# Kernel optimization log

Hardware: AMD Instinct MI355X
Metric: run time of the kernel (lower is better)

Reference implementation:

```python
import jax, jax.numpy as jnp
import numpy as np

K_TOP = 10
DEPTH = 1
N_RULES = 2
N_HOPS = 2
IS_REVERSED = (False, True)


def setup_inputs() -> dict:
    key = jax.random.key(0)
    ks = jax.random.split(key, 11)
    B, E, N, F = 16, 256, 1024, 2048
    return {
        'rel': jax.random.normal(ks[0], (B, E), jnp.float32),
        'arg1': jax.random.normal(ks[1], (B, E), jnp.float32),
        'arg2': jax.random.normal(ks[2], (B, E), jnp.float32),
        'fact_rel': jax.random.normal(ks[3], (B, F, E), jnp.float32),
        'fact_arg1': jax.random.normal(ks[4], (B, F, E), jnp.float32),
        'fact_arg2': jax.random.normal(ks[5], (B, F, E), jnp.float32),
        'nb_facts': jax.random.randint(ks[6], (B,), 1, F + 1),
        'entity_embeddings': jax.random.normal(ks[7], (B, N, E), jnp.float32),
        'nb_entities': jax.random.randint(ks[8], (B,), 1, N + 1),
        'W': jax.random.normal(ks[9], (N_RULES, N_HOPS, E, E), jnp.float32) / np.sqrt(E),
        'b': jnp.zeros((N_RULES, N_HOPS, E), jnp.float32),
    }


def _kernel_scores(q, f):
    # q: [B, M, E], f: [B, F, E] -> Gaussian kernel exp(-0.5*||q-f||^2): [B, M, F]
    d = (jnp.sum(q * q, -1)[..., None] + jnp.sum(f * f, -1)[:, None, :]
         - 2.0 * jnp.einsum('bme,bfe->bmf', q, f))
    return jnp.exp(-0.5 * jnp.maximum(d, 0.0))


def kb_score(rel, arg1, arg2, fact_rel, fact_arg1, fact_arg2, nb_facts):
    # BatchNeuralKB.score: product of per-component kernels, mask padded facts, max over facts.
    B, F, E = fact_rel.shape
    M = rel.shape[0] // B
    r = rel.reshape(B, M, E); a1 = arg1.reshape(B, M, E); a2 = arg2.reshape(B, M, E)
    s = (_kernel_scores(r, fact_rel) * _kernel_scores(a1, fact_arg1)
         * _kernel_scores(a2, fact_arg2))                       # [B, M, F]
    mask = jnp.arange(F)[None, None, :] < nb_facts[:, None, None]
    s = jnp.where(mask, s, 0.0)
    return jnp.max(s, axis=-1).reshape(-1)                      # [B*M]


def prove(rel, arg1, arg2, fact_rel, fact_arg1, fact_arg2, nb_facts,
          entity_embeddings, W, b, depth):
    scores_0 = kb_score(rel, arg1, arg2, fact_rel, fact_arg1, fact_arg2, nb_facts)
    if depth == 0:
        return scores_0
    B, E = rel.shape
    N = entity_embeddings.shape[1]
    global_res = None
    for rule_idx in range(N_RULES):
        is_rev = IS_REVERSED[rule_idx]
        hop_rel_lst = [rel @ W[rule_idx, h] + b[rule_idx, h] for h in range(N_HOPS)]
        sources, scores = arg1, None
        for hop_idx, hop_rel in enumerate(hop_rel_lst, start=1):
            sources_2d = sources.reshape(-1, E)
            nb_branches = sources_2d.shape[0] // B
            hop_rel_2d = jnp.repeat(hop_rel, nb_branches, axis=0)   # [B*br, E]
            if hop_idx < N_HOPS:
                ent_rep = jnp.repeat(entity_embeddings, nb_branches, axis=0)  # [B*br, N, E]
                all_ent_2d = ent_rep.reshape(-1, E)                  # [B*br*N, E]
                new_src_2d = jnp.repeat(sources_2d, N, axis=0)       # [B*br*N, E]
                hop_rel_big = jnp.repeat(hop_rel_2d, N, axis=0)
                na1, na2 = (all_ent_2d, new_src_2d) if is_rev else (new_src_2d, all_ent_2d)
                new_scores = prove(hop_rel_big, na1, na2, fact_rel, fact_arg1,
                                   fact_arg2, nb_facts, entity_embeddings, W, b,
                                   depth - 1).reshape(-1, N)         # [B*br, N]
                k = min(K_TOP, N)
                z_scores, z_idx = jax.lax.top_k(new_scores, k)       # [B*br, k]
                z_emb = jnp.take_along_axis(ent_rep, z_idx[..., None], axis=1)  # [B*br, k, E]
                sources = z_emb.reshape(-1, E)
                z1d = z_scores.reshape(-1)
                scores = z1d if scores is None else jnp.minimum(z1d, jnp.repeat(scores, k))
            else:
                arg2_2d = jnp.repeat(arg2, nb_branches, axis=0)
                na1, na2 = (arg2_2d, sources_2d) if is_rev else (sources_2d, arg2_2d)
                z1d = prove(hop_rel_2d, na1, na2, fact_rel, fact_arg1, fact_arg2,
                            nb_facts, entity_embeddings, W, b, depth - 1)
                scores = z1d if scores is None else jnp.minimum(z1d, scores)
        res = jnp.max(scores.reshape(B, -1), axis=1)
        global_res = res if global_res is None else jnp.maximum(global_res, res)
    return jnp.maximum(scores_0, global_res)


def reference(rel, arg1, arg2, fact_rel, fact_arg1, fact_arg2, nb_facts,
              entity_embeddings, nb_entities, W, b):
    return prove(rel, arg1, arg2, fact_rel, fact_arg1, fact_arg2, nb_facts,
                 entity_embeddings, W, b, depth=DEPTH)
```

## Files before the change

### kernel.cpp

```cpp
#include <hip/hip_runtime.h>
#include <math.h>

#define E 256
#define KTOP 10
#define NY 8
#define NINF (-__builtin_huge_valf())

typedef __attribute__((ext_vector_type(4))) float f32x4;
typedef __attribute__((ext_vector_type(2))) long i64x2;

__device__ inline float wsum(float v) {
    v += __shfl_xor(v, 1, 64);
    v += __shfl_xor(v, 2, 64);
    v += __shfl_xor(v, 4, 64);
    v += __shfl_xor(v, 8, 64);
    v += __shfl_xor(v, 16, 64);
    v += __shfl_xor(v, 32, 64);
    return v;
}

__device__ inline float wmax(float v) {
    v = fmaxf(v, __shfl_xor(v, 1, 64));
    v = fmaxf(v, __shfl_xor(v, 2, 64));
    v = fmaxf(v, __shfl_xor(v, 4, 64));
    v = fmaxf(v, __shfl_xor(v, 8, 64));
    v = fmaxf(v, __shfl_xor(v, 16, 64));
    v = fmaxf(v, __shfl_xor(v, 32, 64));
    return v;
}

__device__ inline float dot4(float4 a, float4 b) {
    return a.x * b.x + a.y * b.y + a.z * b.z + a.w * b.w;
}

__device__ inline void atomicMaxF(float* addr, float v) {
    atomicMax((unsigned int*)addr, __float_as_uint(v));
}

__device__ inline unsigned char f2fp8(float x) {
    unsigned u = __float_as_uint(x);
    unsigned s = (u >> 24) & 0x80u;
    int e = (int)((u >> 23) & 0xFF) - 127;
    unsigned m = u & 0x7FFFFFu;
    if (e < -9) return (unsigned char)s;
    if (e > 8) return (unsigned char)(s | 0x7E);
    if (e >= -6) {
        unsigned mant = m >> 20;
        unsigned rest = m & 0xFFFFFu;
        if (rest > 0x80000u || (rest == 0x80000u && (mant & 1))) mant++;
        unsigned v = (((unsigned)(e + 7)) << 3) + mant;
        if (v > 0x7Eu) v = 0x7Eu;
        return (unsigned char)(s | v);
    }
    int rs = 20 + (-6 - e);
    unsigned full = 0x800000u | m;
    unsigned mant = full >> rs;
    unsigned rem = full & ((1u << rs) - 1u);
    unsigned half = 1u << (rs - 1);
    if (rem > half || (rem == half && (mant & 1))) mant++;
    if (mant >= 8u) return (unsigned char)(s | 0x08u);
    return (unsigned char)(s | mant);
}

__device__ inline int tile_off(int e0, int col) {
    return ((e0 >> 6) << 10) + (col << 6) + (((e0 & 31) >> 3) << 4) +
           (((e0 >> 5) & 1) << 3) + (e0 & 7);
}

__global__ void k_hoprel(const float* __restrict__ rel, const float* __restrict__ arg1,
                         const float* __restrict__ arg2, const float* __restrict__ W,
                         const float* __restrict__ bias, float* __restrict__ hr,
                         float* __restrict__ nhr, float* __restrict__ nrel,
                         float* __restrict__ na1, float* __restrict__ na2, int B) {
    int b = blockIdx.x, rh = blockIdx.y;
    int j = threadIdx.x;
    __shared__ float relS[E];
    __shared__ float red[4];
    __shared__ float red2[4];
    relS[j] = rel[b * E + j];
    __syncthreads();
    const float* Wp = W + (size_t)rh * E * E;
    float acc = bias[rh * E + j];
#pragma unroll 8
    for (int e = 0; e < E; ++e) acc = fmaf(relS[e], Wp[e * E + j], acc);
    hr[((size_t)rh * B + b) * E + j] = acc;
    float s = wsum(acc * acc);
    int wave = j >> 6;
    if ((j & 63) == 0) red[wave] = s;
    float x = 0.f;
    if (rh == 0) x = relS[j];
    else if (rh == 1) x = arg1[b * E + j];
    else if (rh == 2) x = arg2[b * E + j];
    float s2 = wsum(x * x);
    if ((j & 63) == 0) red2[wave] = s2;
    __syncthreads();
    if (j == 0) {
        nhr[rh * B + b] = red[0] + red[1] + red[2] + red[3];
        if (rh < 3) {
            float nv = red2[0] + red2[1] + red2[2] + red2[3];
            (rh == 0 ? nrel : (rh == 1 ? na1 : na2))[b] = nv;
        }
    }
}

__global__ void k_prep_ent(const float* __restrict__ ent, unsigned char* __restrict__ entb,
                           unsigned char* __restrict__ entt, float* __restrict__ ne_,
                           int BN, int N) {
    int row = blockIdx.x * 4 + (threadIdx.x >> 6);
    if (row >= BN) return;
    int lane = threadIdx.x & 63;
    float4 v = ((const float4*)(ent + (size_t)row * E))[lane];
    float s = wsum(dot4(v, v));
    if (lane == 0) ne_[row] = s;
    uchar4 o;
    o.x = f2fp8(v.x); o.y = f2fp8(v.y); o.z = f2fp8(v.z); o.w = f2fp8(v.w);
    ((uchar4*)(entb + (size_t)row * E))[lane] = o;
    int b = row / N, n = row % N;
    size_t tbase = ((size_t)b * (N >> 4) + (n >> 4)) * 4096;
    *(uchar4*)(entt + tbase + tile_off(lane * 4, n & 15)) = o;
}

__global__ __launch_bounds__(256) void k_fused(
    const float* __restrict__ rel, const float* __restrict__ arg1,
    const float* __restrict__ arg2, const float* __restrict__ frel,
    const float* __restrict__ fa1, const float* __restrict__ fa2,
    const int* __restrict__ nbf, const float* __restrict__ hr,
    const float* __restrict__ nhr, const float* __restrict__ nrel,
    const float* __restrict__ na1, const float* __restrict__ na2,
    float* __restrict__ lw1, float* __restrict__ lw2, float* __restrict__ s0log,
    float* __restrict__ nf1, float* __restrict__ nf2,
    unsigned char* __restrict__ fa1b, unsigned char* __restrict__ fa2b,
    int B, int F) {
    int b = blockIdx.y;
    int lane = threadIdx.x & 63, wave = threadIdx.x >> 6;
    int f = blockIdx.x * 4 + wave;
    size_t bf = (size_t)b * F + f;
    float4 qrel = ((const float4*)(rel + (size_t)b * E))[lane];
    float4 qa1  = ((const float4*)(arg1 + (size_t)b * E))[lane];
    float4 qa2  = ((const float4*)(arg2 + (size_t)b * E))[lane];
    float4 qh00 = ((const float4*)(hr + ((size_t)0 * B + b) * E))[lane];
    float4 qh01 = ((const float4*)(hr + ((size_t)1 * B + b) * E))[lane];
    float4 qh10 = ((const float4*)(hr + ((size_t)2 * B + b) * E))[lane];
    float4 qh11 = ((const float4*)(hr + ((size_t)3 * B + b) * E))[lane];
    float4 v  = ((const float4*)(frel + bf * E))[lane];
    float4 v1 = ((const float4*)(fa1 + bf * E))[lane];
    float4 v2 = ((const float4*)(fa2 + bf * E))[lane];
    size_t tbase = ((size_t)b * (F >> 4) + (f >> 4)) * 4096;
    int off = tile_off(lane * 4, f & 15);
    uchar4 c1, c2;
    c1.x = f2fp8(v1.x); c1.y = f2fp8(v1.y); c1.z = f2fp8(v1.z); c1.w = f2fp8(v1.w);
    c2.x = f2fp8(v2.x); c2.y = f2fp8(v2.y); c2.z = f2fp8(v2.z); c2.w = f2fp8(v2.w);
    *(uchar4*)(fa1b + tbase + off) = c1;
    *(uchar4*)(fa2b + tbase + off) = c2;
    float d_rel  = wsum(dot4(v, qrel));
    float d_h00  = wsum(dot4(v, qh00));
    float d_h01  = wsum(dot4(v, qh01));
    float d_h10  = wsum(dot4(v, qh10));
    float d_h11  = wsum(dot4(v, qh11));
    float n_fr   = wsum(dot4(v, v));
    float d_a1f1 = wsum(dot4(v1, qa1));
    float d_a2f1 = wsum(dot4(v1, qa2));
    float n_f1   = wsum(dot4(v1, v1));
    float d_a1f2 = wsum(dot4(v2, qa1));
    float d_a2f2 = wsum(dot4(v2, qa2));
    float n_f2   = wsum(dot4(v2, v2));
    if (lane == 0) {
        bool msk = (f < nbf[b]);
        float rrel  = fmaxf(nrel[b] + n_fr - 2.f * d_rel, 0.f);
        float rh00  = fmaxf(nhr[0 * B + b] + n_fr - 2.f * d_h00, 0.f);
        float rh01  = fmaxf(nhr[1 * B + b] + n_fr - 2.f * d_h01, 0.f);
        float rh10  = fmaxf(nhr[2 * B + b] + n_fr - 2.f * d_h10, 0.f);
        float rh11  = fmaxf(nhr[3 * B + b] + n_fr - 2.f * d_h11, 0.f);
        float ra1f1 = fmaxf(na1[b] + n_f1 - 2.f * d_a1f1, 0.f);
        float ra2f1 = fmaxf(na2[b] + n_f1 - 2.f * d_a2f1, 0.f);
        float ra1f2 = fmaxf(na1[b] + n_f2 - 2.f * d_a1f2, 0.f);
        float ra2f2 = fmaxf(na2[b] + n_f2 - 2.f * d_a2f2, 0.f);
        nf1[bf] = n_f1;
        nf2[bf] = n_f2;
        lw1[bf]                 = msk ? -0.5f * (rh00 + ra1f1) : NINF;
        lw1[(size_t)B * F + bf] = msk ? -0.5f * (rh10 + ra1f2) : NINF;
        lw2[bf]                 = msk ? -0.5f * (rh01 + ra2f2) : NINF;
        lw2[(size_t)B * F + bf] = msk ? -0.5f * (rh11 + ra2f1) : NINF;
        s0log[bf] = msk ? -0.5f * (rrel + ra1f1 + ra2f2) : NINF;
    }
}

__global__ void k_s0red(const float* __restrict__ s0log, float* __restrict__ out,
                        int B, int F) {
    int b = blockIdx.x;
    int tid = threadIdx.x, lane = tid & 63, wave = tid >> 6;
    float m = NINF;
    for (int f = tid; f < F; f += 256) m = fmaxf(m, s0log[(size_t)b * F + f]);
    m = wmax(m);
    __shared__ float red[4];
    if (lane == 0) red[wave] = m;
    __syncthreads();
    if (tid == 0) out[b] = expf(fmaxf(fmaxf(red[0], red[1]), fmaxf(red[2], red[3])));
}

__global__ __launch_bounds__(256, 4) void k_hop1m(
    const unsigned char* __restrict__ entt, const unsigned char* __restrict__ fa1b,
    const unsigned char* __restrict__ fa2b, const float* __restrict__ nf1,
    const float* __restrict__ nf2, const float* __restrict__ ne,
    const float* __restrict__ lw1, float* __restrict__ nsc_part, int B, int N, int F) {
    int L = blockIdx.x;
    int xcd = L & 7, s = L >> 3;
    int b = ((s >> 7) << 3) | xcd;
    int inner = s & 127;
    int r = inner >> 6, nb = (inner >> 3) & 7, fs = inner & 7;
    int BR = nb * 128;
    int F0 = fs * 256;
    const unsigned char* factb = (r == 0) ? fa2b : fa1b;
    const float* nfp = ((r == 0) ? nf2 : nf1) + (size_t)b * F;
    const float* w = lw1 + ((size_t)r * B + b) * F;
    const float* nep = ne + (size_t)b * N;

    __shared__ unsigned char bT[2][4096];

    int tid = threadIdx.x, lane = tid & 63, wave = tid >> 6;
    int lr = lane & 15, lk = lane >> 4;
    int row0 = BR + wave * 32;

    const unsigned char* At = entt + (size_t)b * N * E;
    long areg[2][8];
#pragma unroll
    for (int m = 0; m < 2; ++m) {
        const unsigned char* p = At + (size_t)((row0 >> 4) + m) * 4096 + lr * 64 + lk * 16;
#pragma unroll
        for (int g = 0; g < 4; ++g) {
            i64x2 vv = *(const i64x2*)(p + g * 1024);
            areg[m][2 * g] = vv.x;
            areg[m][2 * g + 1] = vv.y;
        }
    }
    float nh[2][4];
#pragma unroll
    for (int m = 0; m < 2; ++m)
#pragma unroll
        for (int j = 0; j < 4; ++j)
            nh[m][j] = -0.5f * nep[row0 + m * 16 + lk * 4 + j];
    float lwa[16], gfa[16];
#pragma unroll
    for (int t = 0; t < 16; ++t) {
        int fcol = F0 + t * 16 + lr;
        lwa[t] = w[fcol];
        gfa[t] = fmaf(-0.5f, nfp[fcol], lwa[t]);
    }
    float vmax[2][4];
#pragma unroll
    for (int m = 0; m < 2; ++m)
#pragma unroll
        for (int j = 0; j < 4; ++j) vmax[m][j] = NINF;

    const unsigned char* Bt = factb + (size_t)b * F * E + (size_t)(F0 >> 4) * 4096;
#define STG(buf, t)                                                            \
    __builtin_amdgcn_global_load_lds(                                          \
        (const __attribute__((address_space(1))) void*)(Bt + (size_t)(t) * 4096 + \
                                                        wave * 1024 + lane * 16), \
        (__attribute__((address_space(3))) void*)&bT[buf][wave * 1024], 16, 0, 0)

    STG(0, 0);
    __syncthreads();
#pragma unroll
    for (int t = 0; t < 16; ++t) {
        int cur = t & 1;
        if (t < 15) STG(cur ^ 1, t + 1);
        long bfr[8];
#pragma unroll
        for (int g = 0; g < 4; ++g) {
            i64x2 vv = *(const i64x2*)&bT[cur][g * 1024 + lr * 64 + lk * 16];
            bfr[2 * g] = vv.x;
            bfr[2 * g + 1] = vv.y;
        }
        f32x4 acc0 = {0.f, 0.f, 0.f, 0.f}, acc1 = {0.f, 0.f, 0.f, 0.f};
#pragma unroll
        for (int kb = 0; kb < 8; ++kb) {
            acc0 = __builtin_amdgcn_mfma_f32_16x16x32_fp8_fp8(areg[0][kb], bfr[kb],
                                                              acc0, 0, 0, 0);
            acc1 = __builtin_amdgcn_mfma_f32_16x16x32_fp8_fp8(areg[1][kb], bfr[kb],
                                                              acc1, 0, 0, 0);
        }
#pragma unroll
        for (int j = 0; j < 4; ++j) {
            vmax[0][j] = fmaxf(vmax[0][j], fminf(acc0[j] + gfa[t] + nh[0][j], lwa[t]));
            vmax[1][j] = fmaxf(vmax[1][j], fminf(acc1[j] + gfa[t] + nh[1][j], lwa[t]));
        }
        __syncthreads();
    }
#undef STG

#pragma unroll
    for (int m = 0; m < 2; ++m)
#pragma unroll
        for (int j = 0; j < 4; ++j) {
            float v = vmax[m][j];
            v = fmaxf(v, __shfl_xor(v, 1, 64));
            v = fmaxf(v, __shfl_xor(v, 2, 64));
            v = fmaxf(v, __shfl_xor(v, 4, 64));
            v = fmaxf(v, __shfl_xor(v, 8, 64));
            if (lr == 0) {
                int row = row0 + m * 16 + lk * 4 + j;
                nsc_part[(size_t)fs * (2 * (size_t)B * N) +
                         ((size_t)r * B + b) * N + row] = v;
            }
        }
}

__global__ __launch_bounds__(256) void k_topk(const float* __restrict__ nsc_part,
                                              float* __restrict__ zval,
                                              int* __restrict__ zidx, int B, int N) {
    int b = blockIdx.x, r = blockIdx.y;
    int tid = threadIdx.x, lane = tid & 63, wave = tid >> 6;
    size_t rbN = ((size_t)r * B + b) * N;
    size_t ystr = 2 * (size_t)B * N;
    const float4* p0 = (const float4*)(nsc_part + rbN) + tid;
    float4 m = *p0;
#pragma unroll
    for (int y = 1; y < NY; ++y) {
        float4 t = *(const float4*)((const float*)p0 + (size_t)y * ystr);
        m.x = fmaxf(m.x, t.x); m.y = fmaxf(m.y, t.y);
        m.z = fmaxf(m.z, t.z); m.w = fmaxf(m.w, t.w);
    }
    float v0 = expf(m.x), v1 = expf(m.y), v2 = expf(m.z), v3 = expf(m.w);
    int base = tid * 4;
    __shared__ float rv[4];
    __shared__ int ri[4];
    for (int t = 0; t < KTOP; ++t) {
        float bv = v0; int bi = base;
        if (v1 > bv) { bv = v1; bi = base + 1; }
        if (v2 > bv) { bv = v2; bi = base + 2; }
        if (v3 > bv) { bv = v3; bi = base + 3; }
#pragma unroll
        for (int off = 32; off > 0; off >>= 1) {
            float ov = __shfl_xor(bv, off, 64);
            int oi = __shfl_xor(bi, off, 64);
            if (ov > bv || (ov == bv && oi < bi)) { bv = ov; bi = oi; }
        }
        if (lane == 0) { rv[wave] = bv; ri[wave] = bi; }
        __syncthreads();
        float fb = rv[0]; int fi = ri[0];
#pragma unroll
        for (int wv = 1; wv < 4; ++wv) {
            float ov = rv[wv]; int oi = ri[wv];
            if (ov > fb || (ov == fb && oi < fi)) { fb = ov; fi = oi; }
        }
        if (tid == 0) {
            zval[((size_t)r * B + b) * KTOP + t] = fb;
            zidx[((size_t)r * B + b) * KTOP + t] = fi;
        }
        int off = fi - base;
        v0 = (off == 0) ? -2.f : v0;
        v1 = (off == 1) ? -2.f : v1;
        v2 = (off == 2) ? -2.f : v2;
        v3 = (off == 3) ? -2.f : v3;
        __syncthreads();
    }
}

__global__ __launch_bounds__(256) void k_hop2m(
    const unsigned char* __restrict__ entb, const unsigned char* __restrict__ fa1b,
    const unsigned char* __restrict__ fa2b, const float* __restrict__ nf1,
    const float* __restrict__ nf2, const float* __restrict__ ne,
    const float* __restrict__ lw2, const int* __restrict__ zidx,
    float* __restrict__ h2part, int B, int N, int F) {
    int L = blockIdx.x;
    int xcd = L & 7, s = L >> 3;
    int b = ((s >> 4) << 3) | xcd;
    int inner = s & 15;
    int r = inner >> 3, c = inner & 7;
    const unsigned char* factb = (r == 0) ? fa1b : fa2b;
    const float* nfp = ((r == 0) ? nf1 : nf2) + (size_t)b * F;
    const float* w = lw2 + ((size_t)r * B + b) * F;
    int tid = threadIdx.x, lane = tid & 63, wave = tid >> 6;
    int lr = lane & 15, lk = lane >> 4;
    __shared__ unsigned char aLds[32 * 16 * 8];
    __shared__ float snrm[16];
    for (int ci = tid; ci < 512; ci += 256) {
        int row = ci & 15, kc = ci >> 4;
        long vv = 0;
        if (row < KTOP) {
            int idx = zidx[((size_t)r * B + b) * KTOP + row];
            vv = *(const long*)(entb + ((size_t)b * N + idx) * E + kc * 8);
        }
        *(long*)&aLds[(size_t)ci * 8] = vv;
    }
    if (tid < 16) {
        float nv = 0.f;
        if (tid < KTOP) {
            int idx = zidx[((size_t)r * B + b) * KTOP + tid];
            nv = ne[(size_t)b * N + idx];
        }
        snrm[tid] = nv;
    }
    __syncthreads();
    long afr[8];
#pragma unroll
    for (int kb = 0; kb < 8; ++kb)
        afr[kb] = *(const long*)&aLds[((kb * 4 + lk) * 16 + lr) * 8];
    float nhs[4];
#pragma unroll
    for (int j = 0; j < 4; ++j) nhs[j] = -0.5f * snrm[lk * 4 + j];
    int fbase = c * (F >> 3) + wave * (F >> 5);
    float vmax[4] = {NINF, NINF, NINF, NINF};
    const unsigned char* Bb = factb + (size_t)b * F * E;
#pragma unroll
    for (int n = 0; n < 4; ++n) {
        int fcol = fbase + n * 16;
        const unsigned char* p = Bb + (size_t)(fcol >> 4) * 4096 + lr * 64 + lk * 16;
        long bfr[8];
#pragma unroll
        for (int g = 0; g < 4; ++g) {
            i64x2 vv = *(const i64x2*)(p + g * 1024);
            bfr[2 * g] = vv.x;
            bfr[2 * g + 1] = vv.y;
        }
        f32x4 acc = {0.f, 0.f, 0.f, 0.f};
#pragma unroll
        for (int kb = 0; kb < 8; ++kb)
            acc = __builtin_amdgcn_mfma_f32_16x16x32_fp8_fp8(afr[kb], bfr[kb], acc,
                                                             0, 0, 0);
        float lwf = w[fcol + lr];
        float gf = fmaf(-0.5f, nfp[fcol + lr], lwf);
#pragma unroll
        for (int j = 0; j < 4; ++j)
            vmax[j] = fmaxf(vmax[j], fminf(acc[j] + gf + nhs[j], lwf));
    }
#pragma unroll
    for (int j = 0; j < 4; ++j) {
        float v = vmax[j];
        v = fmaxf(v, __shfl_xor(v, 1, 64));
        v = fmaxf(v, __shfl_xor(v, 2, 64));
        v = fmaxf(v, __shfl_xor(v, 4, 64));
        v = fmaxf(v, __shfl_xor(v, 8, 64));
        int sidx = lk * 4 + j;
        if (lr == 0 && sidx < KTOP)
            h2part[(((size_t)r * B + b) * KTOP + sidx) * 32 + c * 4 + wave] = v;
    }
}

__global__ void k_hop2c(const float* __restrict__ h2part, const float* __restrict__ zval,
                        float* __restrict__ out, int B) {
    int i = blockIdx.x * 256 + threadIdx.x;
    int n = 2 * B * KTOP;
    if (i < n) {
        int b = (i / KTOP) % B;
        float m = NINF;
#pragma unroll
        for (int c2 = 0; c2 < 32; ++c2) m = fmaxf(m, h2part[(size_t)i * 32 + c2]);
        float sc = fminf(expf(m), zval[i]);
        atomicMaxF(&out[b], sc);
    }
}

extern "C" void kernel_launch(void* const* d_in, const int* in_sizes, int n_in,
                              void* d_out, int out_size, void* d_ws, size_t ws_size,
                              hipStream_t stream) {
    const float* rel = (const float*)d_in[0];
    const float* arg1 = (const float*)d_in[1];
    const float* arg2 = (const float*)d_in[2];
    const float* frel = (const float*)d_in[3];
    const float* fa1 = (const float*)d_in[4];
    const float* fa2 = (const float*)d_in[5];
    const int* nbf = (const int*)d_in[6];
    const float* ent = (const float*)d_in[7];
    const float* W = (const float*)d_in[9];
    const float* bias = (const float*)d_in[10];
    int B = in_sizes[0] / E;
    int F = in_sizes[3] / (B * E);
    int N = in_sizes[7] / (B * E);
    float* out = (float*)d_out;

    float* ws = (float*)d_ws;
    size_t o = 0;
    float* hr = ws + o;   o += (size_t)4 * B * E;
    float* nhr = ws + o;  o += (size_t)4 * B;
    float* nrel = ws + o; o += B;
    float* na1 = ws + o;  o += B;
    float* na2 = ws + o;  o += B * 2;
    float* nf1 = ws + o;  o += (size_t)B * F;
    float* nf2 = ws + o;  o += (size_t)B * F;
    float* ne_ = ws + o;  o += (size_t)B * N;
    float* lw1 = ws + o;  o += (size_t)2 * B * F;
    float* lw2 = ws + o;  o += (size_t)2 * B * F;
    float* zval = ws + o; o += (size_t)2 * B * KTOP;
    int* zidx = (int*)(ws + o); o += (size_t)2 * B * KTOP;
    float* s0log = ws + o; o += (size_t)B * F;
    float* h2part = ws + o; o += (size_t)2 * B * KTOP * 32;
    float* nsc_part = ws + o; o += (size_t)NY * 2 * B * N;
    unsigned char* fa1b = (unsigned char*)(ws + o); o += (size_t)B * F * E / 4;
    unsigned char* fa2b = (unsigned char*)(ws + o); o += (size_t)B * F * E / 4;
    unsigned char* entb = (unsigned char*)(ws + o); o += (size_t)B * N * E / 4;
    unsigned char* entt = (unsigned char*)(ws + o); o += (size_t)B * N * E / 4;

    k_hoprel<<<dim3(B, 4), dim3(E), 0, stream>>>(rel, arg1, arg2, W, bias, hr, nhr,
                                                 nrel, na1, na2, B);
    k_prep_ent<<<dim3((B * N + 3) / 4), dim3(256), 0, stream>>>(ent, entb, entt, ne_,
                                                                B * N, N);
    k_fused<<<dim3(F / 4, B), dim3(256), 0, stream>>>(
        rel, arg1, arg2, frel, fa1, fa2, nbf, hr, nhr, nrel, na1, na2, lw1, lw2,
        s0log, nf1, nf2, fa1b, fa2b, B, F);
    k_s0red<<<dim3(B), dim3(256), 0, stream>>>(s0log, out, B, F);
    k_hop1m<<<dim3(2048), dim3(256), 0, stream>>>(entt, fa1b, fa2b, nf1, nf2, ne_, lw1,
                                                  nsc_part, B, N, F);
    k_topk<<<dim3(B, 2), dim3(256), 0, stream>>>(nsc_part, zval, zidx, B, N);
    k_hop2m<<<dim3(256), dim3(256), 0, stream>>>(entb, fa1b, fa2b, nf1, nf2, ne_, lw2,
                                                 zidx, h2part, B, N, F);
    k_hop2c<<<dim3((2 * B * KTOP + 255) / 256), dim3(256), 0, stream>>>(h2part, zval,
                                                                        out, B);
}
```

Before: 107.0 us.

## Reorder fp8 tile layout and stage fact conversion through shared memory

The fp8 tile layout now places each lane's 16-byte MFMA fragment contiguously, so a wavefront's fragment loads become consecutive 16-byte chunks in both global memory and LDS. k_fused now handles 16 facts per block, builds the fp8 fact tile in shared memory, and writes it out with coalesced 16-byte stores instead of scattered 4-byte ones. The hop kernels' load addressing is updated to match the new layout. In exchange, k_fused launches a quarter as many blocks and adds a barrier, which reduces available parallelism.

```diff
diff --git a/kernel.cpp b/kernel.cpp
--- a/kernel.cpp
+++ b/kernel.cpp
@@ -63,7 +63,7 @@
 }
 
 __device__ inline int tile_off(int e0, int col) {
-    return ((e0 >> 6) << 10) + (col << 6) + (((e0 & 31) >> 3) << 4) +
+    return ((e0 >> 6) << 10) + (((e0 & 31) >> 3) << 8) + (col << 4) +
            (((e0 >> 5) & 1) << 3) + (e0 & 7);
 }
 
@@ -132,9 +132,10 @@
     unsigned char* __restrict__ fa1b, unsigned char* __restrict__ fa2b,
     int B, int F) {
     int b = blockIdx.y;
-    int lane = threadIdx.x & 63, wave = threadIdx.x >> 6;
-    int f = blockIdx.x * 4 + wave;
-    size_t bf = (size_t)b * F + f;
+    int ft = blockIdx.x;
+    int tid = threadIdx.x, lane = tid & 63, wave = tid >> 6;
+    __shared__ unsigned char l1s[16][288];
+    __shared__ unsigned char l2s[16][288];
     float4 qrel = ((const float4*)(rel + (size_t)b * E))[lane];
     float4 qa1  = ((const float4*)(arg1 + (size_t)b * E))[lane];
     float4 qa2  = ((const float4*)(arg2 + (size_t)b * E))[lane];
@@ -142,46 +143,68 @@
     float4 qh01 = ((const float4*)(hr + ((size_t)1 * B + b) * E))[lane];
     float4 qh10 = ((const float4*)(hr + ((size_t)2 * B + b) * E))[lane];
     float4 qh11 = ((const float4*)(hr + ((size_t)3 * B + b) * E))[lane];
-    float4 v  = ((const float4*)(frel + bf * E))[lane];
-    float4 v1 = ((const float4*)(fa1 + bf * E))[lane];
-    float4 v2 = ((const float4*)(fa2 + bf * E))[lane];
-    size_t tbase = ((size_t)b * (F >> 4) + (f >> 4)) * 4096;
-    int off = tile_off(lane * 4, f & 15);
-    uchar4 c1, c2;
-    c1.x = f2fp8(v1.x); c1.y = f2fp8(v1.y); c1.z = f2fp8(v1.z); c1.w = f2fp8(v1.w);
-    c2.x = f2fp8(v2.x); c2.y = f2fp8(v2.y); c2.z = f2fp8(v2.z); c2.w = f2fp8(v2.w);
-    *(uchar4*)(fa1b + tbase + off) = c1;
-    *(uchar4*)(fa2b + tbase + off) = c2;
-    float d_rel  = wsum(dot4(v, qrel));
-    float d_h00  = wsum(dot4(v, qh00));
-    float d_h01  = wsum(dot4(v, qh01));
-    float d_h10  = wsum(dot4(v, qh10));
-    float d_h11  = wsum(dot4(v, qh11));
-    float n_fr   = wsum(dot4(v, v));
-    float d_a1f1 = wsum(dot4(v1, qa1));
-    float d_a2f1 = wsum(dot4(v1, qa2));
-    float n_f1   = wsum(dot4(v1, v1));
-    float d_a1f2 = wsum(dot4(v2, qa1));
-    float d_a2f2 = wsum(dot4(v2, qa2));
-    float n_f2   = wsum(dot4(v2, v2));
-    if (lane == 0) {
-        bool msk = (f < nbf[b]);
-        float rrel  = fmaxf(nrel[b] + n_fr - 2.f * d_rel, 0.f);
-        float rh00  = fmaxf(nhr[0 * B + b] + n_fr - 2.f * d_h00, 0.f);
-        float rh01  = fmaxf(nhr[1 * B + b] + n_fr - 2.f * d_h01, 0.f);
-        float rh10  = fmaxf(nhr[2 * B + b] + n_fr - 2.f * d_h10, 0.f);
-        float rh11  = fmaxf(nhr[3 * B + b] + n_fr - 2.f * d_h11, 0.f);
-        float ra1f1 = fmaxf(na1[b] + n_f1 - 2.f * d_a1f1, 0.f);
-        float ra2f1 = fmaxf(na2[b] + n_f1 - 2.f * d_a2f1, 0.f);
-        float ra1f2 = fmaxf(na1[b] + n_f2 - 2.f * d_a1f2, 0.f);
-        float ra2f2 = fmaxf(na2[b] + n_f2 - 2.f * d_a2f2, 0.f);
-        nf1[bf] = n_f1;
-        nf2[bf] = n_f2;
-        lw1[bf]                 = msk ? -0.5f * (rh00 + ra1f1) : NINF;
-        lw1[(size_t)B * F + bf] = msk ? -0.5f * (rh10 + ra1f2) : NINF;
-        lw2[bf]                 = msk ? -0.5f * (rh01 + ra2f2) : NINF;
-        lw2[(size_t)B * F + bf] = msk ? -0.5f * (rh11 + ra2f1) : NINF;
-        s0log[bf] = msk ? -0.5f * (rrel + ra1f1 + ra2f2) : NINF;
+    int nbfb = nbf[b];
+    float nrelb = nrel[b], na1b = na1[b], na2b = na2[b];
+    float nh0 = nhr[0 * B + b], nh1 = nhr[1 * B + b];
+    float nh2 = nhr[2 * B + b], nh3 = nhr[3 * B + b];
+#pragma unroll
+    for (int ff = 0; ff < 4; ++ff) {
+        int fr = wave * 4 + ff;
+        int f = ft * 16 + fr;
+        size_t bf = (size_t)b * F + f;
+        float4 v  = ((const float4*)(frel + bf * E))[lane];
+        float4 v1 = ((const float4*)(fa1 + bf * E))[lane];
+        float4 v2 = ((const float4*)(fa2 + bf * E))[lane];
+        uchar4 c1, c2;
+        c1.x = f2fp8(v1.x); c1.y = f2fp8(v1.y); c1.z = f2fp8(v1.z); c1.w = f2fp8(v1.w);
+        c2.x = f2fp8(v2.x); c2.y = f2fp8(v2.y); c2.z = f2fp8(v2.z); c2.w = f2fp8(v2.w);
+        *(uchar4*)&l1s[fr][lane * 4] = c1;
+        *(uchar4*)&l2s[fr][lane * 4] = c2;
+        float d_rel  = wsum(dot4(v, qrel));
+        float d_h00  = wsum(dot4(v, qh00));
+        float d_h01  = wsum(dot4(v, qh01));
+        float d_h10  = wsum(dot4(v, qh10));
+        float d_h11  = wsum(dot4(v, qh11));
+        float n_fr   = wsum(dot4(v, v));
+        float d_a1f1 = wsum(dot4(v1, qa1));
+        float d_a2f1 = wsum(dot4(v1, qa2));
+        float n_f1   = wsum(dot4(v1, v1));
+        float d_a1f2 = wsum(dot4(v2, qa1));
+        float d_a2f2 = wsum(dot4(v2, qa2));
+        float n_f2   = wsum(dot4(v2, v2));
+        if (lane == 0) {
+            bool msk = (f < nbfb);
+            float rrel  = fmaxf(nrelb + n_fr - 2.f * d_rel, 0.f);
+            float rh00  = fmaxf(nh0 + n_fr - 2.f * d_h00, 0.f);
+            float rh01  = fmaxf(nh1 + n_fr - 2.f * d_h01, 0.f);
+            float rh10  = fmaxf(nh2 + n_fr - 2.f * d_h10, 0.f);
+            float rh11  = fmaxf(nh3 + n_fr - 2.f * d_h11, 0.f);
+            float ra1f1 = fmaxf(na1b + n_f1 - 2.f * d_a1f1, 0.f);
+            float ra2f1 = fmaxf(na2b + n_f1 - 2.f * d_a2f1, 0.f);
+            float ra1f2 = fmaxf(na1b + n_f2 - 2.f * d_a1f2, 0.f);
+            float ra2f2 = fmaxf(na2b + n_f2 - 2.f * d_a2f2, 0.f);
+            nf1[bf] = n_f1;
+            nf2[bf] = n_f2;
+            lw1[bf]                 = msk ? -0.5f * (rh00 + ra1f1) : NINF;
+            lw1[(size_t)B * F + bf] = msk ? -0.5f * (rh10 + ra1f2) : NINF;
+            lw2[bf]                 = msk ? -0.5f * (rh01 + ra2f2) : NINF;
+            lw2[(size_t)B * F + bf] = msk ? -0.5f * (rh11 + ra2f1) : NINF;
+            s0log[bf] = msk ? -0.5f * (rrel + ra1f1 + ra2f2) : NINF;
+        }
+    }
+    __syncthreads();
+    {
+        int g = tid >> 6, l = tid & 63;
+        int col = l & 15, lkv = l >> 4;
+        int rowoff = g * 64 + lkv * 8;
+        i64x2 o1, o2;
+        o1.x = *(const long*)&l1s[col][rowoff];
+        o1.y = *(const long*)&l1s[col][rowoff + 32];
+        o2.x = *(const long*)&l2s[col][rowoff];
+        o2.y = *(const long*)&l2s[col][rowoff + 32];
+        size_t tbase = ((size_t)b * (F >> 4) + ft) * 4096;
+        *(i64x2*)(fa1b + tbase + tid * 16) = o1;
+        *(i64x2*)(fa2b + tbase + tid * 16) = o2;
     }
 }
 
@@ -225,7 +248,8 @@
     long areg[2][8];
 #pragma unroll
     for (int m = 0; m < 2; ++m) {
-        const unsigned char* p = At + (size_t)((row0 >> 4) + m) * 4096 + lr * 64 + lk * 16;
+        const unsigned char* p = At + (size_t)((row0 >> 4) + m) * 4096 + lk * 256 +
+                                 lr * 16;
 #pragma unroll
         for (int g = 0; g < 4; ++g) {
             i64x2 vv = *(const i64x2*)(p + g * 1024);
@@ -268,7 +292,7 @@
         long bfr[8];
 #pragma unroll
         for (int g = 0; g < 4; ++g) {
-            i64x2 vv = *(const i64x2*)&bT[cur][g * 1024 + lr * 64 + lk * 16];
+            i64x2 vv = *(const i64x2*)&bT[cur][g * 1024 + lane * 16];
             bfr[2 * g] = vv.x;
             bfr[2 * g + 1] = vv.y;
         }
@@ -406,7 +430,7 @@
 #pragma unroll
     for (int n = 0; n < 4; ++n) {
         int fcol = fbase + n * 16;
-        const unsigned char* p = Bb + (size_t)(fcol >> 4) * 4096 + lr * 64 + lk * 16;
+        const unsigned char* p = Bb + (size_t)(fcol >> 4) * 4096 + lk * 256 + lr * 16;
         long bfr[8];
 #pragma unroll
         for (int g = 0; g < 4; ++g) {
@@ -496,7 +520,7 @@
                                                  nrel, na1, na2, B);
     k_prep_ent<<<dim3((B * N + 3) / 4), dim3(256), 0, stream>>>(ent, entb, entt, ne_,
                                                                 B * N, N);
-    k_fused<<<dim3(F / 4, B), dim3(256), 0, stream>>>(
+    k_fused<<<dim3(F / 16, B), dim3(256), 0, stream>>>(
         rel, arg1, arg2, frel, fa1, fa2, nbf, hr, nhr, nrel, na1, na2, lw1, lw2,
         s0log, nf1, nf2, fa1b, fa2b, B, F);
     k_s0red<<<dim3(B), dim3(256), 0, stream>>>(s0log, out, B, F);
```

Measured after the change: 110.6 us. 3.4% more time.
